# Kernel optimization log

Measured on AMD Instinct MI355X. Metric: run time of the kernel, lower is better.

The kernel has to match this reference:

```python
import jax, jax.numpy as jnp
import numpy as np

EPS = 1e-5  # PyTorch GroupNorm default
NUM_HEADS = 8

def setup_inputs() -> dict:
    key = jax.random.key(0)
    ks = jax.random.split(key, 4)
    B, C, H, W = 16, 256, 32, 32
    x = jax.random.normal(ks[0], (B, C, H, W), dtype=jnp.float32)
    gn_w = jnp.ones((C,), dtype=jnp.float32)
    gn_b = jnp.zeros((C,), dtype=jnp.float32)
    qkv_w = jax.random.normal(ks[1], (3 * C, C), dtype=jnp.float32) * (1.0 / np.sqrt(C))
    qkv_b = jnp.zeros((3 * C,), dtype=jnp.float32)
    proj_w = jax.random.normal(ks[2], (C, C), dtype=jnp.float32) * (1.0 / np.sqrt(C))
    proj_b = jnp.zeros((C,), dtype=jnp.float32)
    return {"x": x, "gn_w": gn_w, "gn_b": gn_b, "qkv_w": qkv_w,
            "qkv_b": qkv_b, "proj_w": proj_w, "proj_b": proj_b}

def reference(x, gn_w, gn_b, qkv_w, qkv_b, proj_w, proj_b):
    b, c, h, w = x.shape
    nh = NUM_HEADS
    hd = c // nh
    scale = hd ** -0.5
    # GroupNorm with 1 group: normalize over (C,H,W) per sample
    mean = jnp.mean(x, axis=(1, 2, 3), keepdims=True)
    var = jnp.var(x, axis=(1, 2, 3), keepdims=True)
    xn = (x - mean) * jax.lax.rsqrt(var + EPS)
    xn = xn * gn_w[None, :, None, None] + gn_b[None, :, None, None]
    # 1x1 conv == per-pixel linear: [b,3c,h,w]
    qkv = jnp.einsum('bchw,oc->bohw', xn, qkv_w) + qkv_b[None, :, None, None]
    qkv = qkv.reshape(b, 3, nh, hd, h * w)          # (b,3,nh,hd,N)
    qkv = jnp.transpose(qkv, (1, 0, 2, 4, 3))       # (3,b,nh,N,hd)
    q, k, v = qkv[0], qkv[1], qkv[2]
    attn = jnp.einsum('bhnd,bhmd->bhnm', q, k) * scale
    attn = jax.nn.softmax(attn, axis=-1)
    out = jnp.einsum('bhnm,bhmd->bhnd', attn, v)     # (b,nh,N,hd)
    out = jnp.transpose(out, (0, 1, 3, 2)).reshape(b, c, h, w)
    out = jnp.einsum('bchw,oc->bohw', out, proj_w) + proj_b[None, :, None, None]
    return out + x
```

## Files before the change

kernel.cpp:

```cpp
#include <hip/hip_runtime.h>
#include <hip/hip_bf16.h>

typedef short bf16x8 __attribute__((ext_vector_type(8)));
typedef float f32x16 __attribute__((ext_vector_type(16)));
typedef unsigned short ushort8 __attribute__((ext_vector_type(8)));
typedef unsigned short ushort4v __attribute__((ext_vector_type(4)));

#define CDIM 256
#define NPIX 1024
#define NB 16
#define NH 8
#define HD 32
#define QSCALE (0.17677669529663687f * 1.4426950408889634f)

static __device__ inline unsigned short f2bf(float f) {
    __hip_bfloat16 h = __float2bfloat16(f);
    return *reinterpret_cast<unsigned short*>(&h);
}

__global__ __launch_bounds__(256)
void gn_partial_kernel(const float* __restrict__ x, float* __restrict__ partial) {
    const int slice = blockIdx.x, b = blockIdx.y;
    const float4* xb = (const float4*)(x + (size_t)b * CDIM * NPIX + slice * 16384);
    const int tid = threadIdx.x;
    float s = 0.f, ss = 0.f;
    #pragma unroll
    for (int i = 0; i < 16; ++i) {
        float4 v = xb[tid + i * 256];
        s  += v.x + v.y + v.z + v.w;
        ss += v.x * v.x + v.y * v.y + v.z * v.z + v.w * v.w;
    }
    __shared__ float r0[256], r1[256];
    r0[tid] = s; r1[tid] = ss;
    __syncthreads();
    for (int st = 128; st > 0; st >>= 1) {
        if (tid < st) { r0[tid] += r0[tid + st]; r1[tid] += r1[tid + st]; }
        __syncthreads();
    }
    if (tid == 0) {
        partial[(b * 16 + slice) * 2 + 0] = r0[0];
        partial[(b * 16 + slice) * 2 + 1] = r1[0];
    }
}

__global__ __launch_bounds__(64)
void gn_final_kernel(const float* __restrict__ partial, float* __restrict__ stats) {
    const int b = blockIdx.x, t = threadIdx.x;
    float s = 0.f, ss = 0.f;
    if (t < 16) { s = partial[(b * 16 + t) * 2]; ss = partial[(b * 16 + t) * 2 + 1]; }
    #pragma unroll
    for (int m = 8; m >= 1; m >>= 1) { s += __shfl_xor(s, m); ss += __shfl_xor(ss, m); }
    if (t == 0) {
        const float inv_n = 1.0f / (float)(CDIM * NPIX);
        float mean = s * inv_n;
        float var  = ss * inv_n - mean * mean;
        stats[b * 2 + 0] = mean;
        stats[b * 2 + 1] = rsqrtf(var + 1e-5f);
    }
}

__global__ __launch_bounds__(256)
void wconv_kernel(const float* __restrict__ qw, const float* __restrict__ pw,
                  unsigned short* __restrict__ wqb, unsigned short* __restrict__ wpb) {
    int idx = blockIdx.x * 256 + threadIdx.x;
    #pragma unroll
    for (int i = 0; i < 4; ++i) {
        int j = idx + i * 65536;
        if (j < 768 * 256) wqb[j] = f2bf(qw[j]);
        else               wpb[j - 768 * 256] = f2bf(pw[j - 768 * 256]);
    }
}

__global__ __launch_bounds__(256)
void xnbt_kernel(const float* __restrict__ x, const float* __restrict__ gnw,
                 const float* __restrict__ gnb, const float* __restrict__ stats,
                 unsigned short* __restrict__ xnbT) {
    const int p0 = blockIdx.x * 64, c0 = blockIdx.y * 64, b = blockIdx.z;
    const int q = threadIdx.x >> 6, l = threadIdx.x & 63;
    const float mean = stats[b * 2], rstd = stats[b * 2 + 1];
    __shared__ float L[64][65];
    const float* xb = x + (size_t)b * CDIM * NPIX;
    #pragma unroll
    for (int i = 0; i < 16; ++i) {
        int ci = q * 16 + i;
        int c = c0 + ci;
        float sc = rstd * gnw[c];
        float sh = gnb[c] - mean * sc;
        L[ci][l] = xb[(size_t)c * NPIX + p0 + l] * sc + sh;
    }
    __syncthreads();
    unsigned short* ob = xnbT + ((size_t)b * NPIX + p0) * CDIM + c0;
    #pragma unroll
    for (int i = 0; i < 16; ++i) {
        int pi = q * 16 + i;
        ob[(size_t)pi * CDIM + l] = f2bf(L[l][pi]);
    }
}

__global__ __launch_bounds__(256)
void qkv_gemm_kernel(const unsigned short* __restrict__ wqb,
                     const float* __restrict__ bias,
                     const unsigned short* __restrict__ xnbT,
                     unsigned short* __restrict__ qkrm,
                     unsigned short* __restrict__ vcm) {
    const int b = blockIdx.z;
    const int m0 = blockIdx.y * 128, p0 = blockIdx.x * 128;
    const int wave = threadIdx.x >> 6, lane = threadIdx.x & 63;
    const int ql = lane & 31, hi = lane >> 5;
    const int wr = wave >> 1, wc = wave & 1;

    const unsigned short* Abase = wqb + (size_t)(m0 + wr * 64) * CDIM;
    const unsigned short* Bbase = xnbT + ((size_t)b * NPIX + p0 + wc * 64) * CDIM;

    f32x16 acc[2][2] = {};
    #pragma unroll
    for (int k0 = 0; k0 < CDIM; k0 += 16) {
        bf16x8 a0 = *(const bf16x8*)(Abase + (size_t)(ql) * CDIM + k0 + hi * 8);
        bf16x8 a1 = *(const bf16x8*)(Abase + (size_t)(32 + ql) * CDIM + k0 + hi * 8);
        bf16x8 b0 = *(const bf16x8*)(Bbase + (size_t)(ql) * CDIM + k0 + hi * 8);
        bf16x8 b1 = *(const bf16x8*)(Bbase + (size_t)(32 + ql) * CDIM + k0 + hi * 8);
        acc[0][0] = __builtin_amdgcn_mfma_f32_32x32x16_bf16(a0, b0, acc[0][0], 0, 0, 0);
        acc[0][1] = __builtin_amdgcn_mfma_f32_32x32x16_bf16(a0, b1, acc[0][1], 0, 0, 0);
        acc[1][0] = __builtin_amdgcn_mfma_f32_32x32x16_bf16(a1, b0, acc[1][0], 0, 0, 0);
        acc[1][1] = __builtin_amdgcn_mfma_f32_32x32x16_bf16(a1, b1, acc[1][1], 0, 0, 0);
    }

    #pragma unroll
    for (int mt = 0; mt < 2; ++mt) {
        const int m_sub = m0 + wr * 64 + mt * 32;
        const int sel = m_sub >> 8;
        const int hh = (m_sub >> 5) & 7;
        #pragma unroll
        for (int pt = 0; pt < 2; ++pt) {
            const int p = p0 + wc * 64 + pt * 32 + ql;
            if (sel < 2) {
                const float qs = (sel == 0) ? QSCALE : 1.0f;
                unsigned short* qk = qkrm + (((size_t)b * 2 + sel) * NH + hh) * NPIX * HD;
                #pragma unroll
                for (int rg = 0; rg < 4; ++rg) {
                    const int dbase = rg * 8 + hi * 4;
                    ushort4v w;
                    #pragma unroll
                    for (int j = 0; j < 4; ++j)
                        w[j] = f2bf((acc[mt][pt][rg * 4 + j] + bias[m_sub + dbase + j]) * qs);
                    *(ushort4v*)(qk + (size_t)p * HD + dbase) = w;
                }
            } else {
                unsigned short* vc = vcm + ((size_t)b * NH + hh) * HD * NPIX;
                #pragma unroll
                for (int r = 0; r < 16; ++r) {
                    const int d = (r & 3) + 8 * (r >> 2) + 4 * hi;
                    vc[(size_t)d * NPIX + p] = f2bf(acc[mt][pt][r] + bias[m_sub + d]);
                }
            }
        }
    }
}

__global__ __launch_bounds__(256)
void attn_mfma_kernel(const unsigned short* __restrict__ qkrm,
                      const unsigned short* __restrict__ vcm,
                      unsigned short* __restrict__ aoutT) {
    const int d = blockIdx.x;
    const int xcd = d & 7, i = d >> 3;
    const int qt = i & 7;
    const int pr = (xcd << 4) | (i >> 3);
    const int h = pr & 7, b = pr >> 3;

    const int tid = threadIdx.x;
    const int wave = tid >> 6, lane = tid & 63;
    const int ql = lane & 31, hi = lane >> 5;
    const int q0 = qt * 128 + wave * 32;

    const unsigned short* Qb = qkrm + (((size_t)b * 2 + 0) * NH + h) * NPIX * HD;
    const unsigned short* Kb = qkrm + (((size_t)b * 2 + 1) * NH + h) * NPIX * HD;
    const unsigned short* Vb = vcm  + ((size_t)b * NH + h) * HD * NPIX;

    __shared__ unsigned short Kl[2][64 * 40];
    __shared__ unsigned short Vl[2][32 * 72];

    bf16x8 qf0 = *(const bf16x8*)(Qb + (size_t)(q0 + ql) * HD + hi * 8);
    bf16x8 qf1 = *(const bf16x8*)(Qb + (size_t)(q0 + ql) * HD + 16 + hi * 8);

    bf16x8 onesv;
    #pragma unroll
    for (int z = 0; z < 8; ++z) onesv[z] = (short)0x3F80;

    f32x16 acc = {};
    f32x16 accl = {};
    float mrun = -1e30f;

    const int krow = tid >> 2, kcol = (tid & 3) * 8;
    const int vrow = tid >> 3, vcol = (tid & 7) * 8;

    ushort8 kreg = *(const ushort8*)(Kb + (size_t)krow * HD + kcol);
    ushort8 vreg = *(const ushort8*)(Vb + (size_t)vrow * NPIX + vcol);
    *(ushort8*)&Kl[0][krow * 40 + kcol] = kreg;
    *(ushort8*)&Vl[0][vrow * 72 + vcol] = vreg;
    kreg = *(const ushort8*)(Kb + (size_t)(64 + krow) * HD + kcol);
    vreg = *(const ushort8*)(Vb + (size_t)vrow * NPIX + 64 + vcol);

    int cur = 0;
    for (int step = 0; step < 16; ++step) {
        __syncthreads();
        if (step + 1 < 16) {
            *(ushort8*)&Kl[cur ^ 1][krow * 40 + kcol] = kreg;
            *(ushort8*)&Vl[cur ^ 1][vrow * 72 + vcol] = vreg;
        }
        if (step + 2 < 16) {
            const int kv = (step + 2) * 64;
            kreg = *(const ushort8*)(Kb + (size_t)(kv + krow) * HD + kcol);
            vreg = *(const ushort8*)(Vb + (size_t)vrow * NPIX + kv + vcol);
        }

        #pragma unroll
        for (int u = 0; u < 2; ++u) {
            const unsigned short* Kr = &Kl[cur][(u * 32 + ql) * 40];
            bf16x8 kf0 = *(const bf16x8*)(Kr + hi * 8);
            bf16x8 kf1 = *(const bf16x8*)(Kr + 16 + hi * 8);
            f32x16 st = {};
            st = __builtin_amdgcn_mfma_f32_32x32x16_bf16(kf0, qf0, st, 0, 0, 0);
            st = __builtin_amdgcn_mfma_f32_32x32x16_bf16(kf1, qf1, st, 0, 0, 0);

            float t0 = fmaxf(fmaxf(st[0], st[1]), st[2]);
            float t1 = fmaxf(fmaxf(st[3], st[4]), st[5]);
            float t2 = fmaxf(fmaxf(st[6], st[7]), st[8]);
            float t3 = fmaxf(fmaxf(st[9], st[10]), st[11]);
            float t4 = fmaxf(fmaxf(st[12], st[13]), st[14]);
            float vmax = fmaxf(fmaxf(fmaxf(t0, t1), t2), fmaxf(fmaxf(t3, t4), st[15]));
            float pmax = fmaxf(vmax, __shfl_xor(vmax, 32));
            if (!__all(pmax - mrun <= 11.5f)) {
                float mnew = fmaxf(mrun, pmax);
                float corr = exp2f(mrun - mnew);
                #pragma unroll
                for (int j = 0; j < 16; ++j) {
                    float cj = __shfl(corr, (j & 3) + 8 * (j >> 2) + 4 * hi);
                    acc[j]  *= cj;
                    accl[j] *= cj;
                }
                mrun = mnew;
            }
            float p[16];
            #pragma unroll
            for (int r = 0; r < 16; ++r) p[r] = exp2f(st[r] - mrun);

            unsigned pk[8];
            #pragma unroll
            for (int k2 = 0; k2 < 8; ++k2) {
                unsigned r_;
                asm("v_cvt_pk_bf16_f32 %0, %1, %2" : "=v"(r_) : "v"(p[2 * k2]), "v"(p[2 * k2 + 1]));
                pk[k2] = r_;
            }
            unsigned x0 = __shfl_xor((int)pk[0], 32), x1 = __shfl_xor((int)pk[1], 32);
            unsigned x2 = __shfl_xor((int)pk[2], 32), x3 = __shfl_xor((int)pk[3], 32);
            unsigned x4 = __shfl_xor((int)pk[4], 32), x5 = __shfl_xor((int)pk[5], 32);
            unsigned x6 = __shfl_xor((int)pk[6], 32), x7 = __shfl_xor((int)pk[7], 32);
            union { unsigned u_[4]; bf16x8 v; } pa0, pa1;
            pa0.u_[0] = hi ? x2    : pk[0];
            pa0.u_[1] = hi ? x3    : pk[1];
            pa0.u_[2] = hi ? pk[2] : x0;
            pa0.u_[3] = hi ? pk[3] : x1;
            pa1.u_[0] = hi ? x6    : pk[4];
            pa1.u_[1] = hi ? x7    : pk[5];
            pa1.u_[2] = hi ? pk[6] : x4;
            pa1.u_[3] = hi ? pk[7] : x5;

            const unsigned short* Vr = &Vl[cur][ql * 72 + u * 32];
            bf16x8 vf0 = *(const bf16x8*)(Vr + hi * 8);
            bf16x8 vf1 = *(const bf16x8*)(Vr + 16 + hi * 8);
            acc  = __builtin_amdgcn_mfma_f32_32x32x16_bf16(pa0.v, vf0, acc, 0, 0, 0);
            acc  = __builtin_amdgcn_mfma_f32_32x32x16_bf16(pa1.v, vf1, acc, 0, 0, 0);
            accl = __builtin_amdgcn_mfma_f32_32x32x16_bf16(pa0.v, onesv, accl, 0, 0, 0);
            accl = __builtin_amdgcn_mfma_f32_32x32x16_bf16(pa1.v, onesv, accl, 0, 0, 0);
        }
        cur ^= 1;
    }

    unsigned short* ob = aoutT + ((size_t)b * NPIX + q0) * CDIM + h * HD;
    #pragma unroll
    for (int j = 0; j < 16; ++j) {
        const int qr = (j & 3) + 8 * (j >> 2) + 4 * hi;
        const float inv_ = 1.0f / accl[j];
        ob[(size_t)qr * CDIM + ql] = f2bf(acc[j] * inv_);
    }
}

__global__ __launch_bounds__(256)
void proj_gemm_kernel(const unsigned short* __restrict__ wpb,
                      const float* __restrict__ bias,
                      const unsigned short* __restrict__ aoutT,
                      const float* __restrict__ xres,
                      float* __restrict__ out) {
    const int b = blockIdx.z;
    const int m0 = blockIdx.y * 128, p0 = blockIdx.x * 128;
    const int wave = threadIdx.x >> 6, lane = threadIdx.x & 63;
    const int ql = lane & 31, hi = lane >> 5;
    const int wr = wave >> 1, wc = wave & 1;

    const unsigned short* Abase = wpb + (size_t)(m0 + wr * 64) * CDIM;
    const unsigned short* Bbase = aoutT + ((size_t)b * NPIX + p0 + wc * 64) * CDIM;

    f32x16 acc[2][2] = {};
    #pragma unroll
    for (int k0 = 0; k0 < CDIM; k0 += 16) {
        bf16x8 a0 = *(const bf16x8*)(Abase + (size_t)(ql) * CDIM + k0 + hi * 8);
        bf16x8 a1 = *(const bf16x8*)(Abase + (size_t)(32 + ql) * CDIM + k0 + hi * 8);
        bf16x8 b0 = *(const bf16x8*)(Bbase + (size_t)(ql) * CDIM + k0 + hi * 8);
        bf16x8 b1 = *(const bf16x8*)(Bbase + (size_t)(32 + ql) * CDIM + k0 + hi * 8);
        acc[0][0] = __builtin_amdgcn_mfma_f32_32x32x16_bf16(a0, b0, acc[0][0], 0, 0, 0);
        acc[0][1] = __builtin_amdgcn_mfma_f32_32x32x16_bf16(a0, b1, acc[0][1], 0, 0, 0);
        acc[1][0] = __builtin_amdgcn_mfma_f32_32x32x16_bf16(a1, b0, acc[1][0], 0, 0, 0);
        acc[1][1] = __builtin_amdgcn_mfma_f32_32x32x16_bf16(a1, b1, acc[1][1], 0, 0, 0);
    }

    #pragma unroll
    for (int mt = 0; mt < 2; ++mt) {
        const int m_sub = m0 + wr * 64 + mt * 32;
        #pragma unroll
        for (int pt = 0; pt < 2; ++pt) {
            const int p = p0 + wc * 64 + pt * 32 + ql;
            #pragma unroll
            for (int r = 0; r < 16; ++r) {
                const int m = m_sub + (r & 3) + 8 * (r >> 2) + 4 * hi;
                const size_t off = ((size_t)b * CDIM + m) * NPIX + p;
                out[off] = acc[mt][pt][r] + bias[m] + xres[off];
            }
        }
    }
}

extern "C" void kernel_launch(void* const* d_in, const int* in_sizes, int n_in,
                              void* d_out, int out_size, void* d_ws, size_t ws_size,
                              hipStream_t stream) {
    const float* x      = (const float*)d_in[0];
    const float* gn_w   = (const float*)d_in[1];
    const float* gn_b   = (const float*)d_in[2];
    const float* qkv_w  = (const float*)d_in[3];
    const float* qkv_b  = (const float*)d_in[4];
    const float* proj_w = (const float*)d_in[5];
    const float* proj_b = (const float*)d_in[6];
    float* out = (float*)d_out;

    char* ws = (char*)d_ws;
    size_t off = 0;
    float* partial = (float*)(ws + off); off += 2048;
    float* stats   = (float*)(ws + off); off += 512;
    unsigned short* wqb  = (unsigned short*)(ws + off); off += (size_t)768 * 256 * 2;
    unsigned short* wpb  = (unsigned short*)(ws + off); off += (size_t)256 * 256 * 2;
    unsigned short* xnbT = (unsigned short*)(ws + off); off += (size_t)NB * NPIX * CDIM * 2;
    unsigned short* qkrm = (unsigned short*)(ws + off); off += (size_t)NB * 2 * NH * NPIX * HD * 2;
    unsigned short* vcm  = (unsigned short*)(ws + off); off += (size_t)NB * NH * HD * NPIX * 2;
    unsigned short* aoutT = (unsigned short*)(ws + off);

    gn_partial_kernel<<<dim3(16, 16), 256, 0, stream>>>(x, partial);
    gn_final_kernel<<<16, 64, 0, stream>>>(partial, stats);
    wconv_kernel<<<256, 256, 0, stream>>>(qkv_w, proj_w, wqb, wpb);
    xnbt_kernel<<<dim3(16, 4, 16), 256, 0, stream>>>(x, gn_w, gn_b, stats, xnbT);

    qkv_gemm_kernel<<<dim3(NPIX / 128, 6, NB), 256, 0, stream>>>(
        wqb, qkv_b, xnbT, qkrm, vcm);

    attn_mfma_kernel<<<1024, 256, 0, stream>>>(qkrm, vcm, aoutT);

    proj_gemm_kernel<<<dim3(NPIX / 128, 2, NB), 256, 0, stream>>>(
        wpb, proj_b, aoutT, x, out);
}
```

Before: 199.7 us.

## Stage GEMM tiles through LDS, split attention KV across two halves, native exp2

Both 1x1-conv GEMMs now go through one templated kernel. It stages 128x64 bf16 tiles of weights and activations in padded shared memory, where the old kernel loaded MFMA fragments straight from global memory. The attention kernel doubles to 512 threads, with each half of the block processing half of the key/value sequence. The two halves' partial softmax states are merged through shared memory at the end. exp2f is replaced by the native exp2 intrinsic, which trades some accuracy for fewer instructions. The costs are extra barriers and LDS traffic in the GEMMs, plus a combine step in attention.

```diff
diff --git a/kernel.cpp b/kernel.cpp
--- a/kernel.cpp
+++ b/kernel.cpp
@@ -12,6 +12,9 @@
 #define NH 8
 #define HD 32
 #define QSCALE (0.17677669529663687f * 1.4426950408889634f)
+
+extern "C" __device__ float __ocml_native_exp2_f32(float);
+#define EXP2N(x) __ocml_native_exp2_f32(x)
 
 static __device__ inline unsigned short f2bf(float f) {
     __hip_bfloat16 h = __float2bfloat16(f);
@@ -97,67 +100,96 @@
     }
 }
 
+template<int EPI>
 __global__ __launch_bounds__(256)
-void qkv_gemm_kernel(const unsigned short* __restrict__ wqb,
-                     const float* __restrict__ bias,
-                     const unsigned short* __restrict__ xnbT,
-                     unsigned short* __restrict__ qkrm,
-                     unsigned short* __restrict__ vcm) {
+void gemm_staged_kernel(const unsigned short* __restrict__ Wb,
+                        const float* __restrict__ bias,
+                        const unsigned short* __restrict__ Bsrc_all,
+                        const float* __restrict__ xres,
+                        float* __restrict__ out,
+                        unsigned short* __restrict__ qkrm,
+                        unsigned short* __restrict__ vcm) {
     const int b = blockIdx.z;
     const int m0 = blockIdx.y * 128, p0 = blockIdx.x * 128;
-    const int wave = threadIdx.x >> 6, lane = threadIdx.x & 63;
+    const int tid = threadIdx.x;
+    const int wave = tid >> 6, lane = tid & 63;
     const int ql = lane & 31, hi = lane >> 5;
     const int wr = wave >> 1, wc = wave & 1;
 
-    const unsigned short* Abase = wqb + (size_t)(m0 + wr * 64) * CDIM;
-    const unsigned short* Bbase = xnbT + ((size_t)b * NPIX + p0 + wc * 64) * CDIM;
+    __shared__ unsigned short As[128 * 72];
+    __shared__ unsigned short Bs[128 * 72];
+
+    const unsigned short* Asrc = Wb + (size_t)m0 * CDIM;
+    const unsigned short* Bsrc = Bsrc_all + ((size_t)b * NPIX + p0) * CDIM;
 
     f32x16 acc[2][2] = {};
-    #pragma unroll
-    for (int k0 = 0; k0 < CDIM; k0 += 16) {
-        bf16x8 a0 = *(const bf16x8*)(Abase + (size_t)(ql) * CDIM + k0 + hi * 8);
-        bf16x8 a1 = *(const bf16x8*)(Abase + (size_t)(32 + ql) * CDIM + k0 + hi * 8);
-        bf16x8 b0 = *(const bf16x8*)(Bbase + (size_t)(ql) * CDIM + k0 + hi * 8);
-        bf16x8 b1 = *(const bf16x8*)(Bbase + (size_t)(32 + ql) * CDIM + k0 + hi * 8);
-        acc[0][0] = __builtin_amdgcn_mfma_f32_32x32x16_bf16(a0, b0, acc[0][0], 0, 0, 0);
-        acc[0][1] = __builtin_amdgcn_mfma_f32_32x32x16_bf16(a0, b1, acc[0][1], 0, 0, 0);
-        acc[1][0] = __builtin_amdgcn_mfma_f32_32x32x16_bf16(a1, b0, acc[1][0], 0, 0, 0);
-        acc[1][1] = __builtin_amdgcn_mfma_f32_32x32x16_bf16(a1, b1, acc[1][1], 0, 0, 0);
+    for (int kc = 0; kc < 4; ++kc) {
+        __syncthreads();
+        #pragma unroll
+        for (int i = 0; i < 4; ++i) {
+            int chunk = i * 256 + tid;
+            int row = chunk >> 3, c8 = chunk & 7;
+            *(ushort8*)&As[row * 72 + c8 * 8] =
+                *(const ushort8*)(Asrc + (size_t)row * CDIM + kc * 64 + c8 * 8);
+            *(ushort8*)&Bs[row * 72 + c8 * 8] =
+                *(const ushort8*)(Bsrc + (size_t)row * CDIM + kc * 64 + c8 * 8);
+        }
+        __syncthreads();
+        #pragma unroll
+        for (int k0 = 0; k0 < 64; k0 += 16) {
+            bf16x8 a0 = *(const bf16x8*)&As[(wr * 64 + ql) * 72 + k0 + hi * 8];
+            bf16x8 a1 = *(const bf16x8*)&As[(wr * 64 + 32 + ql) * 72 + k0 + hi * 8];
+            bf16x8 b0 = *(const bf16x8*)&Bs[(wc * 64 + ql) * 72 + k0 + hi * 8];
+            bf16x8 b1 = *(const bf16x8*)&Bs[(wc * 64 + 32 + ql) * 72 + k0 + hi * 8];
+            acc[0][0] = __builtin_amdgcn_mfma_f32_32x32x16_bf16(a0, b0, acc[0][0], 0, 0, 0);
+            acc[0][1] = __builtin_amdgcn_mfma_f32_32x32x16_bf16(a0, b1, acc[0][1], 0, 0, 0);
+            acc[1][0] = __builtin_amdgcn_mfma_f32_32x32x16_bf16(a1, b0, acc[1][0], 0, 0, 0);
+            acc[1][1] = __builtin_amdgcn_mfma_f32_32x32x16_bf16(a1, b1, acc[1][1], 0, 0, 0);
+        }
     }
 
     #pragma unroll
     for (int mt = 0; mt < 2; ++mt) {
         const int m_sub = m0 + wr * 64 + mt * 32;
-        const int sel = m_sub >> 8;
-        const int hh = (m_sub >> 5) & 7;
         #pragma unroll
         for (int pt = 0; pt < 2; ++pt) {
             const int p = p0 + wc * 64 + pt * 32 + ql;
-            if (sel < 2) {
-                const float qs = (sel == 0) ? QSCALE : 1.0f;
-                unsigned short* qk = qkrm + (((size_t)b * 2 + sel) * NH + hh) * NPIX * HD;
+            if (EPI == 0) {
                 #pragma unroll
-                for (int rg = 0; rg < 4; ++rg) {
-                    const int dbase = rg * 8 + hi * 4;
-                    ushort4v w;
-                    #pragma unroll
-                    for (int j = 0; j < 4; ++j)
-                        w[j] = f2bf((acc[mt][pt][rg * 4 + j] + bias[m_sub + dbase + j]) * qs);
-                    *(ushort4v*)(qk + (size_t)p * HD + dbase) = w;
+                for (int r = 0; r < 16; ++r) {
+                    const int m = m_sub + (r & 3) + 8 * (r >> 2) + 4 * hi;
+                    const size_t off = ((size_t)b * CDIM + m) * NPIX + p;
+                    out[off] = acc[mt][pt][r] + bias[m] + xres[off];
                 }
             } else {
-                unsigned short* vc = vcm + ((size_t)b * NH + hh) * HD * NPIX;
-                #pragma unroll
-                for (int r = 0; r < 16; ++r) {
-                    const int d = (r & 3) + 8 * (r >> 2) + 4 * hi;
-                    vc[(size_t)d * NPIX + p] = f2bf(acc[mt][pt][r] + bias[m_sub + d]);
+                const int sel = m_sub >> 8;
+                const int hh = (m_sub >> 5) & 7;
+                if (sel < 2) {
+                    const float qs = (sel == 0) ? QSCALE : 1.0f;
+                    unsigned short* qk = qkrm + (((size_t)b * 2 + sel) * NH + hh) * NPIX * HD;
+                    #pragma unroll
+                    for (int rg = 0; rg < 4; ++rg) {
+                        const int dbase = rg * 8 + hi * 4;
+                        ushort4v w;
+                        #pragma unroll
+                        for (int j = 0; j < 4; ++j)
+                            w[j] = f2bf((acc[mt][pt][rg * 4 + j] + bias[m_sub + dbase + j]) * qs);
+                        *(ushort4v*)(qk + (size_t)p * HD + dbase) = w;
+                    }
+                } else {
+                    unsigned short* vc = vcm + ((size_t)b * NH + hh) * HD * NPIX;
+                    #pragma unroll
+                    for (int r = 0; r < 16; ++r) {
+                        const int d = (r & 3) + 8 * (r >> 2) + 4 * hi;
+                        vc[(size_t)d * NPIX + p] = f2bf(acc[mt][pt][r] + bias[m_sub + d]);
+                    }
                 }
             }
         }
     }
 }
 
-__global__ __launch_bounds__(256)
+__global__ __launch_bounds__(512)
 void attn_mfma_kernel(const unsigned short* __restrict__ qkrm,
                       const unsigned short* __restrict__ vcm,
                       unsigned short* __restrict__ aoutT) {
@@ -170,15 +202,18 @@
     const int tid = threadIdx.x;
     const int wave = tid >> 6, lane = tid & 63;
     const int ql = lane & 31, hi = lane >> 5;
-    const int q0 = qt * 128 + wave * 32;
+    const int half = tid >> 8;
+    const int wq = wave & 3;
+    const int q0 = qt * 128 + wq * 32;
+    const int kvb = half * 512;
+
+    __shared__ __align__(16) char smem[38912];
+    float* comb = (float*)smem;
 
     const unsigned short* Qb = qkrm + (((size_t)b * 2 + 0) * NH + h) * NPIX * HD;
     const unsigned short* Kb = qkrm + (((size_t)b * 2 + 1) * NH + h) * NPIX * HD;
     const unsigned short* Vb = vcm  + ((size_t)b * NH + h) * HD * NPIX;
 
-    __shared__ unsigned short Kl[2][64 * 40];
-    __shared__ unsigned short Vl[2][32 * 72];
-
     bf16x8 qf0 = *(const bf16x8*)(Qb + (size_t)(q0 + ql) * HD + hi * 8);
     bf16x8 qf1 = *(const bf16x8*)(Qb + (size_t)(q0 + ql) * HD + 16 + hi * 8);
 
@@ -190,25 +225,33 @@
     f32x16 accl = {};
     float mrun = -1e30f;
 
-    const int krow = tid >> 2, kcol = (tid & 3) * 8;
-    const int vrow = tid >> 3, vcol = (tid & 7) * 8;
-
-    ushort8 kreg = *(const ushort8*)(Kb + (size_t)krow * HD + kcol);
-    ushort8 vreg = *(const ushort8*)(Vb + (size_t)vrow * NPIX + vcol);
+    const int t = tid & 255;
+    const int krow = t >> 2, kcol = (t & 3) * 8;
+    const int vrow = t >> 3, vcol = (t & 7) * 8;
+
+    unsigned short* Kl[2];
+    unsigned short* Vl[2];
+    Kl[0] = (unsigned short*)(smem + (half * 2 + 0) * 5120);
+    Kl[1] = (unsigned short*)(smem + (half * 2 + 1) * 5120);
+    Vl[0] = (unsigned short*)(smem + 20480 + (half * 2 + 0) * 4608);
+    Vl[1] = (unsigned short*)(smem + 20480 + (half * 2 + 1) * 4608);
+
+    ushort8 kreg = *(const ushort8*)(Kb + (size_t)(kvb + krow) * HD + kcol);
+    ushort8 vreg = *(const ushort8*)(Vb + (size_t)vrow * NPIX + kvb + vcol);
     *(ushort8*)&Kl[0][krow * 40 + kcol] = kreg;
     *(ushort8*)&Vl[0][vrow * 72 + vcol] = vreg;
-    kreg = *(const ushort8*)(Kb + (size_t)(64 + krow) * HD + kcol);
-    vreg = *(const ushort8*)(Vb + (size_t)vrow * NPIX + 64 + vcol);
+    kreg = *(const ushort8*)(Kb + (size_t)(kvb + 64 + krow) * HD + kcol);
+    vreg = *(const ushort8*)(Vb + (size_t)vrow * NPIX + kvb + 64 + vcol);
 
     int cur = 0;
-    for (int step = 0; step < 16; ++step) {
+    for (int step = 0; step < 8; ++step) {
         __syncthreads();
-        if (step + 1 < 16) {
+        if (step + 1 < 8) {
             *(ushort8*)&Kl[cur ^ 1][krow * 40 + kcol] = kreg;
             *(ushort8*)&Vl[cur ^ 1][vrow * 72 + vcol] = vreg;
         }
-        if (step + 2 < 16) {
-            const int kv = (step + 2) * 64;
+        if (step + 2 < 8) {
+            const int kv = kvb + (step + 2) * 64;
             kreg = *(const ushort8*)(Kb + (size_t)(kv + krow) * HD + kcol);
             vreg = *(const ushort8*)(Vb + (size_t)vrow * NPIX + kv + vcol);
         }
@@ -231,7 +274,7 @@
             float pmax = fmaxf(vmax, __shfl_xor(vmax, 32));
             if (!__all(pmax - mrun <= 11.5f)) {
                 float mnew = fmaxf(mrun, pmax);
-                float corr = exp2f(mrun - mnew);
+                float corr = EXP2N(mrun - mnew);
                 #pragma unroll
                 for (int j = 0; j < 16; ++j) {
                     float cj = __shfl(corr, (j & 3) + 8 * (j >> 2) + 4 * hi);
@@ -242,7 +285,7 @@
             }
             float p[16];
             #pragma unroll
-            for (int r = 0; r < 16; ++r) p[r] = exp2f(st[r] - mrun);
+            for (int r = 0; r < 16; ++r) p[r] = EXP2N(st[r] - mrun);
 
             unsigned pk[8];
             #pragma unroll
@@ -276,55 +319,31 @@
         cur ^= 1;
     }
 
-    unsigned short* ob = aoutT + ((size_t)b * NPIX + q0) * CDIM + h * HD;
-    #pragma unroll
-    for (int j = 0; j < 16; ++j) {
-        const int qr = (j & 3) + 8 * (j >> 2) + 4 * hi;
-        const float inv_ = 1.0f / accl[j];
-        ob[(size_t)qr * CDIM + ql] = f2bf(acc[j] * inv_);
-    }
-}
-
-__global__ __launch_bounds__(256)
-void proj_gemm_kernel(const unsigned short* __restrict__ wpb,
-                      const float* __restrict__ bias,
-                      const unsigned short* __restrict__ aoutT,
-                      const float* __restrict__ xres,
-                      float* __restrict__ out) {
-    const int b = blockIdx.z;
-    const int m0 = blockIdx.y * 128, p0 = blockIdx.x * 128;
-    const int wave = threadIdx.x >> 6, lane = threadIdx.x & 63;
-    const int ql = lane & 31, hi = lane >> 5;
-    const int wr = wave >> 1, wc = wave & 1;
-
-    const unsigned short* Abase = wpb + (size_t)(m0 + wr * 64) * CDIM;
-    const unsigned short* Bbase = aoutT + ((size_t)b * NPIX + p0 + wc * 64) * CDIM;
-
-    f32x16 acc[2][2] = {};
-    #pragma unroll
-    for (int k0 = 0; k0 < CDIM; k0 += 16) {
-        bf16x8 a0 = *(const bf16x8*)(Abase + (size_t)(ql) * CDIM + k0 + hi * 8);
-        bf16x8 a1 = *(const bf16x8*)(Abase + (size_t)(32 + ql) * CDIM + k0 + hi * 8);
-        bf16x8 b0 = *(const bf16x8*)(Bbase + (size_t)(ql) * CDIM + k0 + hi * 8);
-        bf16x8 b1 = *(const bf16x8*)(Bbase + (size_t)(32 + ql) * CDIM + k0 + hi * 8);
-        acc[0][0] = __builtin_amdgcn_mfma_f32_32x32x16_bf16(a0, b0, acc[0][0], 0, 0, 0);
-        acc[0][1] = __builtin_amdgcn_mfma_f32_32x32x16_bf16(a0, b1, acc[0][1], 0, 0, 0);
-        acc[1][0] = __builtin_amdgcn_mfma_f32_32x32x16_bf16(a1, b0, acc[1][0], 0, 0, 0);
-        acc[1][1] = __builtin_amdgcn_mfma_f32_32x32x16_bf16(a1, b1, acc[1][1], 0, 0, 0);
-    }
-
-    #pragma unroll
-    for (int mt = 0; mt < 2; ++mt) {
-        const int m_sub = m0 + wr * 64 + mt * 32;
-        #pragma unroll
-        for (int pt = 0; pt < 2; ++pt) {
-            const int p = p0 + wc * 64 + pt * 32 + ql;
-            #pragma unroll
-            for (int r = 0; r < 16; ++r) {
-                const int m = m_sub + (r & 3) + 8 * (r >> 2) + 4 * hi;
-                const size_t off = ((size_t)b * CDIM + m) * NPIX + p;
-                out[off] = acc[mt][pt][r] + bias[m] + xres[off];
-            }
+    __syncthreads();
+    if (half == 1) {
+        float* cb = comb + ((size_t)wq * 64 + lane) * 33;
+        #pragma unroll
+        for (int j = 0; j < 16; ++j) cb[j] = acc[j];
+        #pragma unroll
+        for (int j = 0; j < 16; ++j) cb[16 + j] = accl[j];
+        cb[32] = mrun;
+    }
+    __syncthreads();
+    if (half == 0) {
+        const float* cb = comb + ((size_t)wq * 64 + lane) * 33;
+        float m1 = cb[32];
+        float mstar = fmaxf(mrun, m1);
+        float f0 = EXP2N(mrun - mstar);
+        float f1 = EXP2N(m1 - mstar);
+        unsigned short* ob = aoutT + ((size_t)b * NPIX + q0) * CDIM + h * HD;
+        #pragma unroll
+        for (int j = 0; j < 16; ++j) {
+            const int qr = (j & 3) + 8 * (j >> 2) + 4 * hi;
+            float f0j = __shfl(f0, qr);
+            float f1j = __shfl(f1, qr);
+            float a  = acc[j]  * f0j + cb[j]      * f1j;
+            float l  = accl[j] * f0j + cb[16 + j] * f1j;
+            ob[(size_t)qr * CDIM + ql] = f2bf(a * (1.0f / l));
         }
     }
 }
@@ -357,11 +376,11 @@
     wconv_kernel<<<256, 256, 0, stream>>>(qkv_w, proj_w, wqb, wpb);
     xnbt_kernel<<<dim3(16, 4, 16), 256, 0, stream>>>(x, gn_w, gn_b, stats, xnbT);
 
-    qkv_gemm_kernel<<<dim3(NPIX / 128, 6, NB), 256, 0, stream>>>(
-        wqb, qkv_b, xnbT, qkrm, vcm);
-
-    attn_mfma_kernel<<<1024, 256, 0, stream>>>(qkrm, vcm, aoutT);
-
-    proj_gemm_kernel<<<dim3(NPIX / 128, 2, NB), 256, 0, stream>>>(
-        wpb, proj_b, aoutT, x, out);
-}
+    gemm_staged_kernel<1><<<dim3(NPIX / 128, 6, NB), 256, 0, stream>>>(
+        wqb, qkv_b, xnbT, nullptr, nullptr, qkrm, vcm);
+
+    attn_mfma_kernel<<<1024, 512, 0, stream>>>(qkrm, vcm, aoutT);
+
+    gemm_staged_kernel<0><<<dim3(NPIX / 128, 2, NB), 256, 0, stream>>>(
+        wpb, proj_b, aoutT, x, out, nullptr, nullptr);
+}
```

Result: faster. 194.4 us (-2.7%).
